# Kernel tuning notes

Hardware: AMD Instinct MI355X
Metric: run time of the kernel (lower is better)

## Reference

```python
import jax, jax.numpy as jnp
import numpy as np

B = 8192
DIMS = [5, 1024, 1024, 512, 512, 512, 512, 2]  # model_param
L1, L2, OBS_X, OBS_Y, R = 3.0, 3.0, 0.0, 7.0, 4.0


def _linear_params(key, fan_in, fan_out):
    kw, kb = jax.random.split(key)
    lim = 1.0 / np.sqrt(fan_in)
    W = jax.random.uniform(kw, (fan_in, fan_out), jnp.float32, -lim, lim)
    b = jax.random.uniform(kb, (fan_out,), jnp.float32, -lim, lim)
    return W, b


def setup_inputs() -> dict:
    key = jax.random.key(0)
    keys = jax.random.split(key, 9)
    x = jax.random.normal(keys[0], (B, DIMS[0]), jnp.float32)
    W1, b1 = _linear_params(keys[1], DIMS[0], DIMS[1])
    W2, b2 = _linear_params(keys[2], DIMS[1], DIMS[2])
    W31, b31 = _linear_params(keys[3], DIMS[2], DIMS[3])
    W32, b32 = _linear_params(keys[4], DIMS[2], DIMS[4])
    W41, b41 = _linear_params(keys[5], DIMS[3], DIMS[5])
    W42, b42 = _linear_params(keys[6], DIMS[4], DIMS[6])
    W51, b51 = _linear_params(keys[7], DIMS[5], DIMS[7])
    W52, b52 = _linear_params(keys[8], DIMS[6], DIMS[7])
    return {
        'x': x, 'sgn': 1,
        'mean': jnp.zeros((DIMS[0],), jnp.float32),
        'std': jnp.ones((DIMS[0],), jnp.float32),
        'mean_label': jnp.zeros((2,), jnp.float32),
        'std_label': jnp.ones((2,), jnp.float32),
        'W1': W1, 'b1': b1, 'W2': W2, 'b2': b2,
        'W31': W31, 'b31': b31, 'W32': W32, 'b32': b32,
        'W41': W41, 'b41': b41, 'W42': W42, 'b42': b42,
        'W51': W51, 'b51': b51, 'W52': W52, 'b52': b52,
    }


def _forward(x, mean, std, mean_label, std_label,
             W1, b1, W2, b2, W31, b31, W32, b32,
             W41, b41, W42, b42, W51, b51, W52, b52):
    act = jax.nn.relu
    x0 = x * std + mean                      # un-normalized state [B,5]
    x1 = act(x @ W1 + b1)
    x2 = act(x1 @ W2 + b2)
    x31 = act(x2 @ W31 + b31)
    x32 = act(x2 @ W32 + b32)
    x41 = act(x31 @ W41 + b41)
    x42 = act(x32 @ W42 + b42)
    x51 = x41 @ W51 + b51                    # QP linear term p  [B,2]
    x52 = 4.0 * jax.nn.sigmoid(x42 @ W52 + b52)  # CBF class-K gains [B,2]

    # dCBF terms (two-link arm obstacle barrier)
    t1, w1, t2, w2 = x0[:, 0], x0[:, 1], x0[:, 2], x0[:, 3]
    s1, s2, c1, c2 = jnp.sin(t1), jnp.sin(t2), jnp.cos(t1), jnp.cos(t2)
    px = L1 * c1 + L2 * c2 - OBS_X
    py = L1 * s1 + L2 * s2 - OBS_Y
    vx = -L1 * s1 * w1 - L2 * s2 * w2
    vy = L1 * c1 * w1 + L2 * c2 * w2
    barrier = px * px + py * py - R * R
    b_dot = 2.0 * (px * vx + py * vy)
    Lf2b = (2.0 * (vx * vx + vy * vy)
            + 2.0 * px * (-L1 * c1 * w1 * w1 - L2 * c2 * w2 * w2)
            + 2.0 * py * (-L1 * s1 * w1 * w1 - L2 * s2 * w2 * w2))
    # G (single inequality row, 2 columns), G u <= h
    G1 = -(2.0 * px * (-L1 * s1) + 2.0 * py * (L1 * c1))
    G2 = -(2.0 * px * (-L2 * s2) + 2.0 * py * (L2 * c2))
    G = jnp.stack([G1, G2], axis=1)          # [B,2]
    h = Lf2b + (x52[:, 0] + x52[:, 1]) * b_dot + x52[:, 0] * x52[:, 1] * barrier  # [B]

    # QP: min 0.5||u||^2 + x51.u  s.t. G u <= h  -> closed-form KKT projection
    u0 = -x51                                 # unconstrained optimum
    viol = jnp.sum(G * u0, axis=1) - h        # [B]
    lam = jnp.maximum(viol, 0.0) / (jnp.sum(G * G, axis=1) + 1e-12)
    u = u0 - lam[:, None] * G                 # [B,2]
    return (u - mean_label) / std_label


def reference(x, sgn, mean, std, mean_label, std_label,
              W1, b1, W2, b2, W31, b31, W32, b32,
              W41, b41, W42, b42, W51, b51, W52, b52):
    # sgn == 1 -> batched QP branch (the trained/deployed path)
    return _forward(x, mean, std, mean_label, std_label,
                    W1, b1, W2, b2, W31, b31, W32, b32,
                    W41, b41, W42, b42, W51, b51, W52, b52)
```

## Files before the change

### kernel.cpp

```cpp
#include <hip/hip_runtime.h>
#include <hip/hip_bf16.h>
#include <math.h>


typedef __attribute__((ext_vector_type(4))) float f32x4;
typedef __attribute__((ext_vector_type(8))) short bf16x8;

static __device__ __forceinline__ unsigned short f2bf(float f) {
    unsigned int u = __float_as_uint(f);
    unsigned int r = (u + 0x7fffu + ((u >> 16) & 1u)) >> 16;
    return (unsigned short)r;
}
static __device__ __forceinline__ float bf2f(unsigned short h) {
    return __uint_as_float(((unsigned int)h) << 16);
}

#define TM 128
#define TN 128
#define TK 32

#define GLL(gp, lp) __builtin_amdgcn_global_load_lds( \
    (const __attribute__((address_space(1))) void*)(gp), \
    (__attribute__((address_space(3))) void*)(lp), 16, 0, 0)

#define LGKM0() asm volatile("s_waitcnt lgkmcnt(0)" ::: "memory")
#define VMC(N)  asm volatile("s_waitcnt vmcnt(" #N ")" ::: "memory")
#define BAR()   __builtin_amdgcn_s_barrier()
#define SB0()   __builtin_amdgcn_sched_barrier(0)

__device__ __forceinline__ void gemm_core(
    const unsigned short* __restrict__ A, int lda,
    const unsigned short* __restrict__ Bt, int ldb,
    const float* __restrict__ bias,
    unsigned short* __restrict__ C, int ldc,
    int K, int m0, int n0b, int c0)
{
    __shared__ __align__(16) short sA0[TM * TK], sB0v[TN * TK];
    __shared__ __align__(16) short sA1[TM * TK], sB1v[TN * TK];

    const int tid  = threadIdx.x;
    const int w    = tid >> 6;
    const int lane = tid & 63;

    const unsigned short* aG =
        A + (size_t)(m0 + w * 32 + (lane >> 2)) * lda + (lane & 3) * 8;
    const unsigned short* bG =
        Bt + (size_t)(n0b + w * 32 + (lane >> 2)) * ldb + (lane & 3) * 8;

    const int wr = (w >> 1) * 64;
    const int wc = (w & 1) * 64;
    const int fr = lane & 15;
    const int fq = lane >> 4;

    f32x4 acc[4][4] = {};
    const int nt = K / TK;

    auto STAGE = [&](int kt, short* la, short* lb) {
        const unsigned short* a0 = aG + (size_t)kt * TK;
        const unsigned short* b0 = bG + (size_t)kt * TK;
        GLL(a0,            la + w * 1024);
        GLL(a0 + 16 * lda, la + w * 1024 + 512);
        GLL(b0,            lb + w * 1024);
        GLL(b0 + 16 * ldb, lb + w * 1024 + 512);
    };

    auto BODY = [&](int t, short* sAp, short* sBp) {
        bf16x8 af[4], bf[4];
        #pragma unroll
        for (int m = 0; m < 4; ++m)
            af[m] = *reinterpret_cast<const bf16x8*>(
                &sAp[(wr + m * 16 + fr) * TK + fq * 8]);
        #pragma unroll
        for (int n = 0; n < 4; ++n)
            bf[n] = *reinterpret_cast<const bf16x8*>(
                &sBp[(wc + n * 16 + fr) * TK + fq * 8]);
        LGKM0();
        BAR();
        SB0();
        if (t + 2 < nt) STAGE(t + 2, sAp, sBp);
        #pragma unroll
        for (int m = 0; m < 4; ++m)
            #pragma unroll
            for (int n = 0; n < 4; ++n)
                acc[m][n] = __builtin_amdgcn_mfma_f32_16x16x32_bf16(
                    af[m], bf[n], acc[m][n], 0, 0, 0);
        if (t + 1 < nt) {
            if (t + 2 < nt) { VMC(4); } else { VMC(0); }
            BAR();
            SB0();
        }
    };

    STAGE(0, sA0, sB0v);
    STAGE(1, sA1, sB1v);
    VMC(4);
    BAR();
    SB0();

    for (int t = 0; t < nt; t += 2) {
        BODY(t,     sA0, sB0v);
        BODY(t + 1, sA1, sB1v);
    }

    #pragma unroll
    for (int n = 0; n < 4; ++n) {
        const int cl = wc + n * 16 + fr;
        const float bv = bias[n0b + cl];
        #pragma unroll
        for (int m = 0; m < 4; ++m) {
            const int rbase = m0 + wr + m * 16 + fq * 4;
            #pragma unroll
            for (int r = 0; r < 4; ++r) {
                float v = fmaxf(acc[m][n][r] + bv, 0.0f);
                C[(size_t)(rbase + r) * ldc + c0 + cl] = f2bf(v);
            }
        }
    }
}

__global__ __launch_bounds__(256) void gemm_bf16(
    const unsigned short* __restrict__ A, int lda,
    const unsigned short* __restrict__ Bt, int ldb,
    const float* __restrict__ bias,
    unsigned short* __restrict__ C, int ldc, int K)
{
    const int n0 = blockIdx.x * TN;
    const int m0 = blockIdx.y * TM;
    gemm_core(A, lda, Bt, ldb, bias, C, ldc, K, m0, n0, n0);
}

__global__ __launch_bounds__(256) void gemm_bf16_l4(
    const unsigned short* __restrict__ x3,
    const unsigned short* __restrict__ W41t,
    const unsigned short* __restrict__ W42t,
    const float* __restrict__ b41, const float* __restrict__ b42,
    unsigned short* __restrict__ x4)
{
    const int g   = blockIdx.x >> 2;
    const int n0b = (blockIdx.x & 3) * TN;
    const int m0  = blockIdx.y * TM;
    const unsigned short* A  = x3 + (g ? 512 : 0);
    const unsigned short* Bt = g ? W42t : W41t;
    const float* bias        = g ? b42 : b41;
    gemm_core(A, 1024, Bt, 512, bias, x4, 1024, 512, m0, n0b, g * 512 + n0b);
}

__global__ __launch_bounds__(256) void prep_weights(
    const float* __restrict__ W2,  const float* __restrict__ W31,
    const float* __restrict__ W32, const float* __restrict__ W41,
    const float* __restrict__ W42, const float* __restrict__ b31,
    const float* __restrict__ b32,
    unsigned short* __restrict__ W2t,  unsigned short* __restrict__ W3t,
    unsigned short* __restrict__ W41t, unsigned short* __restrict__ W42t,
    float* __restrict__ b3c)
{
    const int z = blockIdx.z;
    if (z == 5) {
        if (blockIdx.x == 0 && blockIdx.y == 0) {
            for (int i = threadIdx.x; i < 1024; i += 256)
                b3c[i] = (i < 512) ? b31[i] : b32[i - 512];
        }
        return;
    }
    const float* src; unsigned short* dst; int K, N;
    switch (z) {
        case 0:  src = W2;  dst = W2t;              K = 1024; N = 1024; break;
        case 1:  src = W31; dst = W3t;              K = 1024; N = 512;  break;
        case 2:  src = W32; dst = W3t + 512 * 1024; K = 1024; N = 512;  break;
        case 3:  src = W41; dst = W41t;             K = 512;  N = 512;  break;
        default: src = W42; dst = W42t;             K = 512;  N = 512;  break;
    }
    const int k0 = blockIdx.x * 32, n0 = blockIdx.y * 32;
    if (k0 >= K || n0 >= N) return;

    __shared__ float t[32][33];
    const int tx = threadIdx.x & 31, ty = threadIdx.x >> 5;
    #pragma unroll
    for (int i = 0; i < 32; i += 8)
        t[ty + i][tx] = src[(size_t)(k0 + ty + i) * N + n0 + tx];
    __syncthreads();
    #pragma unroll
    for (int i = 0; i < 32; i += 8)
        dst[(size_t)(n0 + ty + i) * K + k0 + tx] = f2bf(t[tx][ty + i]);
}

__global__ __launch_bounds__(256) void layer1_kernel(
    const float* __restrict__ x, const float* __restrict__ W1,
    const float* __restrict__ b1, unsigned short* __restrict__ x1out)
{
    const int row = blockIdx.x;
    const int j4 = threadIdx.x * 4;
    float xr[5];
    #pragma unroll
    for (int k = 0; k < 5; ++k) xr[k] = x[row * 5 + k];
    float4 acc = *reinterpret_cast<const float4*>(&b1[j4]);
    #pragma unroll
    for (int k = 0; k < 5; ++k) {
        float4 wv = *reinterpret_cast<const float4*>(&W1[k * 1024 + j4]);
        acc.x = fmaf(xr[k], wv.x, acc.x);
        acc.y = fmaf(xr[k], wv.y, acc.y);
        acc.z = fmaf(xr[k], wv.z, acc.z);
        acc.w = fmaf(xr[k], wv.w, acc.w);
    }
    ushort4 o;
    o.x = f2bf(fmaxf(acc.x, 0.f));
    o.y = f2bf(fmaxf(acc.y, 0.f));
    o.z = f2bf(fmaxf(acc.z, 0.f));
    o.w = f2bf(fmaxf(acc.w, 0.f));
    *reinterpret_cast<ushort4*>(&x1out[(size_t)row * 1024 + j4]) = o;
}

__global__ __launch_bounds__(256) void head_kernel(
    const unsigned short* __restrict__ x4,
    const float* __restrict__ W51, const float* __restrict__ b51,
    const float* __restrict__ W52, const float* __restrict__ b52,
    const float* __restrict__ x,   const float* __restrict__ mean,
    const float* __restrict__ stdv, const float* __restrict__ mean_label,
    const float* __restrict__ std_label, float* __restrict__ out)
{
    const int wave = threadIdx.x >> 6;
    const int lane = threadIdx.x & 63;
    const int row = blockIdx.x * 4 + wave;

    const unsigned short* p41 = x4 + (size_t)row * 1024;
    const unsigned short* p42 = p41 + 512;

    float a0 = 0.f, a1 = 0.f, a2 = 0.f, a3 = 0.f;
    #pragma unroll
    for (int it = 0; it < 8; ++it) {
        const int k = lane + it * 64;
        const float v1 = bf2f(p41[k]);
        const float2 w5 = *reinterpret_cast<const float2*>(&W51[k * 2]);
        a0 = fmaf(v1, w5.x, a0);
        a1 = fmaf(v1, w5.y, a1);
        const float v2 = bf2f(p42[k]);
        const float2 w6 = *reinterpret_cast<const float2*>(&W52[k * 2]);
        a2 = fmaf(v2, w6.x, a2);
        a3 = fmaf(v2, w6.y, a3);
    }
    #pragma unroll
    for (int off = 32; off >= 1; off >>= 1) {
        a0 += __shfl_down(a0, off);
        a1 += __shfl_down(a1, off);
        a2 += __shfl_down(a2, off);
        a3 += __shfl_down(a3, off);
    }

    if (lane == 0) {
        const float L1c = 3.0f, L2c = 3.0f, OBSX = 0.0f, OBSY = 7.0f, Rc = 4.0f;
        const float t1 = x[row * 5 + 0] * stdv[0] + mean[0];
        const float w1 = x[row * 5 + 1] * stdv[1] + mean[1];
        const float t2 = x[row * 5 + 2] * stdv[2] + mean[2];
        const float w2 = x[row * 5 + 3] * stdv[3] + mean[3];
        const float s1 = sinf(t1), c1 = cosf(t1);
        const float s2 = sinf(t2), c2 = cosf(t2);
        const float px = L1c * c1 + L2c * c2 - OBSX;
        const float py = L1c * s1 + L2c * s2 - OBSY;
        const float vx = -L1c * s1 * w1 - L2c * s2 * w2;
        const float vy =  L1c * c1 * w1 + L2c * c2 * w2;
        const float barrier = px * px + py * py - Rc * Rc;
        const float b_dot = 2.0f * (px * vx + py * vy);
        const float Lf2b = 2.0f * (vx * vx + vy * vy)
                         + 2.0f * px * (-L1c * c1 * w1 * w1 - L2c * c2 * w2 * w2)
                         + 2.0f * py * (-L1c * s1 * w1 * w1 - L2c * s2 * w2 * w2);
        const float G1 = -(2.0f * px * (-L1c * s1) + 2.0f * py * (L1c * c1));
        const float G2 = -(2.0f * px * (-L2c * s2) + 2.0f * py * (L2c * c2));

        const float x51_0 = a0 + b51[0];
        const float x51_1 = a1 + b51[1];
        const float z0 = a2 + b52[0];
        const float z1 = a3 + b52[1];
        const float x52_0 = 4.0f / (1.0f + expf(-z0));
        const float x52_1 = 4.0f / (1.0f + expf(-z1));

        const float u0_0 = -x51_0;
        const float u0_1 = -x51_1;
        const float h = Lf2b + (x52_0 + x52_1) * b_dot + x52_0 * x52_1 * barrier;
        const float viol = G1 * u0_0 + G2 * u0_1 - h;
        const float lam = fmaxf(viol, 0.0f) / (G1 * G1 + G2 * G2 + 1e-12f);
        const float u_0 = u0_0 - lam * G1;
        const float u_1 = u0_1 - lam * G2;
        out[row * 2 + 0] = (u_0 - mean_label[0]) / std_label[0];
        out[row * 2 + 1] = (u_1 - mean_label[1]) / std_label[1];
    }
}

extern "C" void kernel_launch(void* const* d_in, const int* in_sizes, int n_in,
                              void* d_out, int out_size, void* d_ws, size_t ws_size,
                              hipStream_t stream) {
    const float* x          = (const float*)d_in[0];
    const float* mean       = (const float*)d_in[2];
    const float* stdv       = (const float*)d_in[3];
    const float* mean_label = (const float*)d_in[4];
    const float* std_label  = (const float*)d_in[5];
    const float* W1  = (const float*)d_in[6];   const float* b1  = (const float*)d_in[7];
    const float* W2  = (const float*)d_in[8];   const float* b2  = (const float*)d_in[9];
    const float* W31 = (const float*)d_in[10];  const float* b31 = (const float*)d_in[11];
    const float* W32 = (const float*)d_in[12];  const float* b32 = (const float*)d_in[13];
    const float* W41 = (const float*)d_in[14];  const float* b41 = (const float*)d_in[15];
    const float* W42 = (const float*)d_in[16];  const float* b42 = (const float*)d_in[17];
    const float* W51 = (const float*)d_in[18];  const float* b51 = (const float*)d_in[19];
    const float* W52 = (const float*)d_in[20];  const float* b52 = (const float*)d_in[21];
    float* out = (float*)d_out;

    char* ws = (char*)d_ws;
    const size_t MiB = 1024 * 1024;
    unsigned short* xb1  = (unsigned short*)(ws + 0);
    unsigned short* x2b  = (unsigned short*)(ws + 16 * MiB);
    unsigned short* x3   = xb1;
    unsigned short* x4   = x2b;
    unsigned short* W2t  = (unsigned short*)(ws + 32 * MiB);
    unsigned short* W3t  = (unsigned short*)(ws + 34 * MiB);
    unsigned short* W41t = (unsigned short*)(ws + 36 * MiB);
    unsigned short* W42t = (unsigned short*)(ws + 36 * MiB + 512 * 1024);
    float*          b3c  = (float*)(ws + 37 * MiB);

    prep_weights<<<dim3(32, 32, 6), 256, 0, stream>>>(
        W2, W31, W32, W41, W42, b31, b32, W2t, W3t, W41t, W42t, b3c);

    layer1_kernel<<<8192, 256, 0, stream>>>(x, W1, b1, xb1);

    dim3 gL2(1024 / TN, 8192 / TM);
    gemm_bf16<<<gL2, 256, 0, stream>>>(xb1, 1024, W2t, 1024, b2, x2b, 1024, 1024);
    gemm_bf16<<<gL2, 256, 0, stream>>>(x2b, 1024, W3t, 1024, b3c, x3, 1024, 1024);

    gemm_bf16_l4<<<dim3(8, 64), 256, 0, stream>>>(x3, W41t, W42t, b41, b42, x4);

    head_kernel<<<2048, 256, 0, stream>>>(x4, W51, b51, W52, b52,
                                          x, mean, stdv, mean_label, std_label, out);
}
```

Baseline: 98.44 us.

## Enlarge GEMM tiles to 128x256x64 with 8 waves and XOR-swizzled LDS

The bf16 GEMM core moves from 128x128x32 tiles with 4 waves to 128x256x64 tiles with 8 waves per block. An XOR swizzle is applied to the LDS layout to avoid bank conflicts on fragment reads. Each barrier now covers twice as many MFMAs and the larger tile raises operand reuse. In exchange, LDS use grows to 96 KB per block and the grids shrink to 256 blocks, which may lower occupancy and CU balance on a 256-CU device.

```diff
diff --git a/kernel.cpp b/kernel.cpp
--- a/kernel.cpp
+++ b/kernel.cpp
@@ -15,9 +15,9 @@
     return __uint_as_float(((unsigned int)h) << 16);
 }
 
-#define TM 128
-#define TN 128
-#define TK 32
+#define TBM 128
+#define TBN 256
+#define TBK 64
 
 #define GLL(gp, lp) __builtin_amdgcn_global_load_lds( \
     (const __attribute__((address_space(1))) void*)(gp), \
@@ -35,57 +35,72 @@
     unsigned short* __restrict__ C, int ldc,
     int K, int m0, int n0b, int c0)
 {
-    __shared__ __align__(16) short sA0[TM * TK], sB0v[TN * TK];
-    __shared__ __align__(16) short sA1[TM * TK], sB1v[TN * TK];
+    __shared__ __align__(16) short sA0[TBM * TBK], sA1[TBM * TBK];
+    __shared__ __align__(16) short sB0v[TBN * TBK], sB1v[TBN * TBK];
 
     const int tid  = threadIdx.x;
     const int w    = tid >> 6;
     const int lane = tid & 63;
 
-    const unsigned short* aG =
-        A + (size_t)(m0 + w * 32 + (lane >> 2)) * lda + (lane & 3) * 8;
-    const unsigned short* bG =
-        Bt + (size_t)(n0b + w * 32 + (lane >> 2)) * ldb + (lane & 3) * 8;
-
-    const int wr = (w >> 1) * 64;
-    const int wc = (w & 1) * 64;
+    const int srow = lane >> 3;
+    const int skq  = (lane & 7) ^ ((lane >> 3) & 7);
+    const unsigned short* aP0 =
+        A + (size_t)(m0 + 16 * w + srow) * lda + skq * 8;
+    const unsigned short* aP1 = aP0 + 8 * lda;
+    const unsigned short* bP0 =
+        Bt + (size_t)(n0b + 32 * w + srow) * ldb + skq * 8;
+    const unsigned short* bP1 = bP0 + 8 * ldb;
+    const unsigned short* bP2 = bP0 + 16 * ldb;
+    const unsigned short* bP3 = bP0 + 24 * ldb;
+
+    const int wrow = (w >> 2) * 64;
+    const int wcol = (w & 3) * 64;
     const int fr = lane & 15;
     const int fq = lane >> 4;
+    const int swz0 = ((fq)     ^ (fr & 7)) * 8;
+    const int swz1 = ((4 + fq) ^ (fr & 7)) * 8;
 
     f32x4 acc[4][4] = {};
-    const int nt = K / TK;
+    const int nt = K / TBK;
 
     auto STAGE = [&](int kt, short* la, short* lb) {
-        const unsigned short* a0 = aG + (size_t)kt * TK;
-        const unsigned short* b0 = bG + (size_t)kt * TK;
-        GLL(a0,            la + w * 1024);
-        GLL(a0 + 16 * lda, la + w * 1024 + 512);
-        GLL(b0,            lb + w * 1024);
-        GLL(b0 + 16 * ldb, lb + w * 1024 + 512);
+        const size_t ko = (size_t)kt * TBK;
+        GLL(aP0 + ko, la + (2 * w)     * 512);
+        GLL(aP1 + ko, la + (2 * w + 1) * 512);
+        GLL(bP0 + ko, lb + (4 * w)     * 512);
+        GLL(bP1 + ko, lb + (4 * w + 1) * 512);
+        GLL(bP2 + ko, lb + (4 * w + 2) * 512);
+        GLL(bP3 + ko, lb + (4 * w + 3) * 512);
     };
 
     auto BODY = [&](int t, short* sAp, short* sBp) {
-        bf16x8 af[4], bf[4];
+        bf16x8 af[2][4], bf[2][4];
         #pragma unroll
-        for (int m = 0; m < 4; ++m)
-            af[m] = *reinterpret_cast<const bf16x8*>(
-                &sAp[(wr + m * 16 + fr) * TK + fq * 8]);
+        for (int m = 0; m < 4; ++m) {
+            const int r = (wrow + m * 16 + fr) * 64;
+            af[0][m] = *reinterpret_cast<const bf16x8*>(&sAp[r + swz0]);
+            af[1][m] = *reinterpret_cast<const bf16x8*>(&sAp[r + swz1]);
+        }
         #pragma unroll
-        for (int n = 0; n < 4; ++n)
-            bf[n] = *reinterpret_cast<const bf16x8*>(
-                &sBp[(wc + n * 16 + fr) * TK + fq * 8]);
+        for (int n = 0; n < 4; ++n) {
+            const int r = (wcol + n * 16 + fr) * 64;
+            bf[0][n] = *reinterpret_cast<const bf16x8*>(&sBp[r + swz0]);
+            bf[1][n] = *reinterpret_cast<const bf16x8*>(&sBp[r + swz1]);
+        }
         LGKM0();
         BAR();
         SB0();
         if (t + 2 < nt) STAGE(t + 2, sAp, sBp);
         #pragma unroll
-        for (int m = 0; m < 4; ++m)
+        for (int kh = 0; kh < 2; ++kh)
             #pragma unroll
-            for (int n = 0; n < 4; ++n)
-                acc[m][n] = __builtin_amdgcn_mfma_f32_16x16x32_bf16(
-                    af[m], bf[n], acc[m][n], 0, 0, 0);
+            for (int m = 0; m < 4; ++m)
+                #pragma unroll
+                for (int n = 0; n < 4; ++n)
+                    acc[m][n] = __builtin_amdgcn_mfma_f32_16x16x32_bf16(
+                        af[kh][m], bf[kh][n], acc[m][n], 0, 0, 0);
         if (t + 1 < nt) {
-            if (t + 2 < nt) { VMC(4); } else { VMC(0); }
+            if (t + 2 < nt) { VMC(6); } else { VMC(0); }
             BAR();
             SB0();
         }
@@ -93,7 +108,7 @@
 
     STAGE(0, sA0, sB0v);
     STAGE(1, sA1, sB1v);
-    VMC(4);
+    VMC(6);
     BAR();
     SB0();
 
@@ -104,11 +119,11 @@
 
     #pragma unroll
     for (int n = 0; n < 4; ++n) {
-        const int cl = wc + n * 16 + fr;
+        const int cl = wcol + n * 16 + fr;
         const float bv = bias[n0b + cl];
         #pragma unroll
         for (int m = 0; m < 4; ++m) {
-            const int rbase = m0 + wr + m * 16 + fq * 4;
+            const int rbase = m0 + wrow + m * 16 + fq * 4;
             #pragma unroll
             for (int r = 0; r < 4; ++r) {
                 float v = fmaxf(acc[m][n][r] + bv, 0.0f);
@@ -118,27 +133,27 @@
     }
 }
 
-__global__ __launch_bounds__(256) void gemm_bf16(
+__global__ __launch_bounds__(512, 2) void gemm_bf16(
     const unsigned short* __restrict__ A, int lda,
     const unsigned short* __restrict__ Bt, int ldb,
     const float* __restrict__ bias,
     unsigned short* __restrict__ C, int ldc, int K)
 {
-    const int n0 = blockIdx.x * TN;
-    const int m0 = blockIdx.y * TM;
+    const int n0 = blockIdx.x * TBN;
+    const int m0 = blockIdx.y * TBM;
     gemm_core(A, lda, Bt, ldb, bias, C, ldc, K, m0, n0, n0);
 }
 
-__global__ __launch_bounds__(256) void gemm_bf16_l4(
+__global__ __launch_bounds__(512, 2) void gemm_bf16_l4(
     const unsigned short* __restrict__ x3,
     const unsigned short* __restrict__ W41t,
     const unsigned short* __restrict__ W42t,
     const float* __restrict__ b41, const float* __restrict__ b42,
     unsigned short* __restrict__ x4)
 {
-    const int g   = blockIdx.x >> 2;
-    const int n0b = (blockIdx.x & 3) * TN;
-    const int m0  = blockIdx.y * TM;
+    const int g   = blockIdx.x >> 1;
+    const int n0b = (blockIdx.x & 1) * TBN;
+    const int m0  = blockIdx.y * TBM;
     const unsigned short* A  = x3 + (g ? 512 : 0);
     const unsigned short* Bt = g ? W42t : W41t;
     const float* bias        = g ? b42 : b41;
@@ -320,11 +335,11 @@
 
     layer1_kernel<<<8192, 256, 0, stream>>>(x, W1, b1, xb1);
 
-    dim3 gL2(1024 / TN, 8192 / TM);
-    gemm_bf16<<<gL2, 256, 0, stream>>>(xb1, 1024, W2t, 1024, b2, x2b, 1024, 1024);
-    gemm_bf16<<<gL2, 256, 0, stream>>>(x2b, 1024, W3t, 1024, b3c, x3, 1024, 1024);
-
-    gemm_bf16_l4<<<dim3(8, 64), 256, 0, stream>>>(x3, W41t, W42t, b41, b42, x4);
+    dim3 gBig(1024 / TBN, 8192 / TBM);
+    gemm_bf16<<<gBig, 512, 0, stream>>>(xb1, 1024, W2t, 1024, b2, x2b, 1024, 1024);
+    gemm_bf16<<<gBig, 512, 0, stream>>>(x2b, 1024, W3t, 1024, b3c, x3, 1024, 1024);
+
+    gemm_bf16_l4<<<dim3(4, 64), 512, 0, stream>>>(x3, W41t, W42t, b41, b42, x4);
 
     head_kernel<<<2048, 256, 0, stream>>>(x4, W51, b51, W52, b52,
                                           x, mean, stdv, mean_label, std_label, out);
```

New measurement: 88.86 us. 1.11x faster.
